# Performance work log

Measured on AMD Instinct MI355X. Metric: run time of the kernel, lower is better.

The kernel has to match this reference:

```python
import jax, jax.numpy as jnp
import numpy as np

N_NODES = 50000
N_EDGES = 600000
N_GRAPHS = 64
IN_D, HID, EMB = 5, 128, 64
BN_EPS = 1e-5


def setup_inputs() -> dict:
    key = jax.random.key(0)
    ks = jax.random.split(key, 16)
    x = jax.random.normal(ks[0], (N_NODES, IN_D), dtype=jnp.float32)
    src = jax.random.randint(ks[1], (N_EDGES,), 0, N_NODES, dtype=jnp.int32)
    dst = jax.random.randint(ks[2], (N_EDGES,), 0, N_NODES, dtype=jnp.int32)
    batch = jnp.sort(jax.random.randint(ks[3], (N_NODES,), 0, N_GRAPHS, dtype=jnp.int32))
    def lin(k, fi, fo):
        s = 1.0 / np.sqrt(fi)
        kw, kb = jax.random.split(k)
        return (jax.random.uniform(kw, (fi, fo), jnp.float32, -s, s),
                jax.random.uniform(kb, (fo,), jnp.float32, -s, s))
    W1, b1 = lin(ks[4], IN_D, HID)
    W2, b2 = lin(ks[5], HID, HID)
    W3, b3 = lin(ks[6], HID, HID)
    Wp, bp = lin(ks[7], HID, EMB)
    g1 = 1.0 + 0.1 * jax.random.normal(ks[8], (HID,), jnp.float32)
    g2 = 1.0 + 0.1 * jax.random.normal(ks[9], (HID,), jnp.float32)
    g3 = 1.0 + 0.1 * jax.random.normal(ks[10], (HID,), jnp.float32)
    be1 = 0.1 * jax.random.normal(ks[11], (HID,), jnp.float32)
    be2 = 0.1 * jax.random.normal(ks[12], (HID,), jnp.float32)
    be3 = 0.1 * jax.random.normal(ks[13], (HID,), jnp.float32)
    return dict(x=x, src=src, dst=dst, batch=batch,
                W1=W1, b1=b1, W2=W2, b2=b2, W3=W3, b3=b3,
                g1=g1, be1=be1, g2=g2, be2=be2, g3=g3, be3=be3,
                Wp=Wp, bp=bp)


def reference(x, src, dst, batch, W1, b1, W2, b2, W3, b3,
              g1, be1, g2, be2, g3, be3, Wp, bp):
    n = x.shape[0]
    # GCNConv with self-loops and symmetric normalization (PyG default)
    loop = jnp.arange(n, dtype=src.dtype)
    s = jnp.concatenate([src, loop])
    d = jnp.concatenate([dst, loop])
    deg = jax.ops.segment_sum(jnp.ones_like(d, dtype=x.dtype), d, num_segments=n)
    dinv = jnp.where(deg > 0, jax.lax.rsqrt(deg), 0.0)
    norm = (dinv[s] * dinv[d])[:, None]  # (E+N, 1)

    def gcn(h, W, b):
        hw = h @ W                                   # (N, HID)
        msg = hw[s] * norm                           # gather + scale
        agg = jax.ops.segment_sum(msg, d, num_segments=n)
        return agg + b

    def bn_relu(h, g, be):
        # eval-mode BatchNorm1d with running_mean=0, running_var=1
        return jax.nn.relu(h * (g * jax.lax.rsqrt(jnp.asarray(1.0 + BN_EPS, h.dtype))) + be)

    h = bn_relu(gcn(x, W1, b1), g1, be1)
    h = bn_relu(gcn(h, W2, b2), g2, be2)
    h = bn_relu(gcn(h, W3, b3), g3, be3)

    # global mean pool over graphs
    sums = jax.ops.segment_sum(h, batch, num_segments=N_GRAPHS)
    cnt = jax.ops.segment_sum(jnp.ones((n,), h.dtype), batch, num_segments=N_GRAPHS)
    pooled = sums / jnp.maximum(cnt, 1.0)[:, None]
    return pooled @ Wp + bp
```

## Files before the change

### kernel.cpp

```cpp
#include <hip/hip_runtime.h>
#include <hip/hip_fp16.h>

#define N_NODES 50000
#define N_EDGES 600000
#define N_GRAPHS 64
#define IN_D 5
#define HID 128
#define EMB 64

#define CHUNK 512
#define NCHUNK ((N_NODES + CHUNK - 1) / CHUNK)
#define NREP 16
#define NLOC 4
#define TB 16
#define ECAP 1024

typedef _Float16 half8 __attribute__((ext_vector_type(8)));
typedef float float4v __attribute__((ext_vector_type(4)));
typedef float floatx2 __attribute__((ext_vector_type(2)));


__global__ __launch_bounds__(256) void k_init(
        int* __restrict__ cnt, float* __restrict__ psum_rep,
        const float* __restrict__ W2, const float* __restrict__ W3,
        _Float16* __restrict__ Wt2, _Float16* __restrict__ Wt3,
        int2* __restrict__ e_pack,
        const float* __restrict__ x, float* __restrict__ xp) {
    int tid = blockIdx.x * blockDim.x + threadIdx.x;
    int nt = gridDim.x * blockDim.x;
    for (int i = tid; i < N_NODES; i += nt) cnt[i] = 0;
    for (int i = tid; i < NREP * N_GRAPHS * HID; i += nt) psum_rep[i] = 0.f;
    if (tid < 8) e_pack[N_EDGES + tid] = make_int2(0, 0);
    for (int i = tid; i < N_NODES * 8; i += nt) {
        int f = i & 7, n = i >> 3;
        xp[i] = (f < IN_D) ? x[n * IN_D + f] : 0.f;
    }
    for (int i = tid; i < 2 * HID * HID; i += nt) {
        int rem = i & (HID * HID - 1);
        int k = rem & 127, f = rem >> 7;
        if (i < HID * HID) Wt2[rem] = (_Float16)W2[k * HID + f];
        else               Wt3[rem] = (_Float16)W3[k * HID + f];
    }
}


__global__ __launch_bounds__(256) void k_count(
        const int* __restrict__ dst, int* __restrict__ cnt) {
    int e = blockIdx.x * blockDim.x + threadIdx.x;
    if (e < N_EDGES) atomicAdd(&cnt[dst[e]], 1);
}


__global__ void k_chunksum(const int* __restrict__ cnt, int* __restrict__ csum,
                           float* __restrict__ dinv) {
    __shared__ int sh[256];
    int b = blockIdx.x, t = threadIdx.x;
    int i0 = b * CHUNK + t, i1 = i0 + 256;
    int v = 0;
    if (i0 < N_NODES) { int c = cnt[i0]; v += c; dinv[i0] = rsqrtf((float)c + 1.0f); }
    if (i1 < N_NODES) { int c = cnt[i1]; v += c; dinv[i1] = rsqrtf((float)c + 1.0f); }
    sh[t] = v; __syncthreads();
    for (int off = 128; off > 0; off >>= 1) {
        if (t < off) sh[t] += sh[t + off];
        __syncthreads();
    }
    if (t == 0) csum[b] = sh[0];
}


__global__ void k_scan(const int* __restrict__ cnt, const int* __restrict__ csum,
                       int* __restrict__ row_start) {
    __shared__ int ws[4];
    int b = blockIdx.x, t = threadIdx.x;
    int lane = t & 63, w = t >> 6;

    int pre = 0;
    for (int j = lane; j < b; j += 64) pre += csum[j];
    #pragma unroll
    for (int off = 32; off > 0; off >>= 1) pre += __shfl_down(pre, off);
    pre = __shfl(pre, 0);

    int base = b * CHUNK;
    int i0 = base + 2 * t, i1 = i0 + 1;
    int c0 = (i0 < N_NODES) ? cnt[i0] : 0;
    int c1 = (i1 < N_NODES) ? cnt[i1] : 0;
    int v = c0 + c1;
    int s = v;
    #pragma unroll
    for (int off = 1; off < 64; off <<= 1) {
        int u = __shfl_up(s, off);
        if (lane >= off) s += u;
    }
    if (lane == 63) ws[w] = s;
    __syncthreads();
    if (t == 0) {
        int r = 0;
        #pragma unroll
        for (int j = 0; j < 4; ++j) { int xx = ws[j]; ws[j] = r; r += xx; }
    }
    __syncthreads();
    int excl = s - v + ws[w] + pre;
    if (i0 < N_NODES) row_start[i0] = excl;
    if (i1 < N_NODES) row_start[i1] = excl + c0;
    if (b == 0 && t == 0) row_start[N_NODES] = N_EDGES;
}


__global__ __launch_bounds__(256) void k_scatter(
        const int* __restrict__ src, const int* __restrict__ dst,
        const float* __restrict__ dinv, const int* __restrict__ row_start,
        int* __restrict__ cnt, int2* __restrict__ e_pack) {
    int e = blockIdx.x * blockDim.x + threadIdx.x;
    if (e >= N_EDGES) return;
    int d = dst[e];
    int pos = row_start[d] + atomicSub(&cnt[d], 1) - 1;
    int s = src[e];
    e_pack[pos] = make_int2(s, __float_as_int(dinv[s]));
}


__global__ __launch_bounds__(256) void k_agg1(
        const float* __restrict__ xp, const float* __restrict__ dinv,
        const int* __restrict__ row_start, const int2* __restrict__ e_pack,
        const float* __restrict__ W1, const float* __restrict__ b1,
        const float* __restrict__ g1, const float* __restrict__ be1,
        unsigned short* __restrict__ H8u) {
    __shared__ int2 eL[ECAP];
    int t = threadIdx.x;
    int w = t >> 6, lane = t & 63;
    int slot8 = lane >> 3, q8 = lane & 7;
    int nb = blockIdx.x * TB;

    int E0 = row_start[nb], E1 = row_start[nb + TB];
    int cntL = E1 - E0 + 8; if (cntL > ECAP) cntL = ECAP;
    for (int i = t; i < cntL; i += 256) eL[i] = e_pack[E0 + i];
    __syncthreads();

    const float rs = rsqrtf(1.0f + 1e-5f);
    int fa = lane * 2, fb = fa + 1;
    float w1a[IN_D], w1b[IN_D];
    #pragma unroll
    for (int k = 0; k < IN_D; ++k) {
        w1a[k] = W1[k * HID + fa];
        w1b[k] = W1[k * HID + fb];
    }
    float b1a = b1[fa], b1b = b1[fb];
    float g1a = g1[fa] * rs, g1b = g1[fb] * rs;
    float e1a = be1[fa], e1b = be1[fb];

    #pragma unroll 1
    for (int i = 0; i < 4; ++i) {
        int n = nb + w * 4 + i;
        int beg = row_start[n], end = row_start[n + 1];
        float acc = 0.f;
        for (int e = beg; e < end; e += 8) {
            int eo = e + slot8 - E0;
            int2 pe;
            if (eo < cntL) pe = eL[eo];
            else           pe = e_pack[e + slot8];
            float fw = (e + slot8 < end) ? __int_as_float(pe.y) : 0.f;
            float g = xp[(size_t)pe.x * 8 + q8];
            acc = fmaf(fw, g, acc);
        }
        acc += __shfl_xor(acc, 8);
        acc += __shfl_xor(acc, 16);
        acc += __shfl_xor(acc, 32);
        float di = dinv[n];
        float av = di * fmaf(di, xp[(size_t)n * 8 + q8], acc);
        float a0 = __shfl(av, 0), a1 = __shfl(av, 1), a2 = __shfl(av, 2),
              a3 = __shfl(av, 3), a4 = __shfl(av, 4);
        float va = b1a, vb = b1b;
        va = fmaf(a0, w1a[0], va); vb = fmaf(a0, w1b[0], vb);
        va = fmaf(a1, w1a[1], va); vb = fmaf(a1, w1b[1], vb);
        va = fmaf(a2, w1a[2], va); vb = fmaf(a2, w1b[2], vb);
        va = fmaf(a3, w1a[3], va); vb = fmaf(a3, w1b[3], vb);
        va = fmaf(a4, w1a[4], va); vb = fmaf(a4, w1b[4], vb);
        va = fmaf(va, g1a, e1a);
        vb = fmaf(vb, g1b, e1b);
        va = va > 0.f ? va : 0.f;
        vb = vb > 0.f ? vb : 0.f;
        int p = __builtin_amdgcn_cvt_pk_fp8_f32(va, vb, 0, false);
        H8u[(size_t)n * 64 + lane] = (unsigned short)(p & 0xffff);
    }
}


__device__ __forceinline__ void agg_node_fp8(
        const unsigned int* __restrict__ H8, const float* __restrict__ dinv,
        const int* __restrict__ row_start, const int2* __restrict__ e_pack,
        const int2* __restrict__ eL, int E0, int cntL,
        int n, int slot8, int q8, _Float16* __restrict__ asrow) {
    float acc[16];
    #pragma unroll
    for (int j = 0; j < 16; ++j) acc[j] = 0.f;
    int beg = row_start[n], end = row_start[n + 1];
    for (int e = beg; e < end; e += 8) {
        int eo = e + slot8 - E0;
        int2 pe;
        if (eo < cntL) pe = eL[eo];
        else           pe = e_pack[e + slot8];
        float fw = (e + slot8 < end) ? __int_as_float(pe.y) : 0.f;
        uint4 g = ((const uint4*)(H8 + (size_t)pe.x * 32))[q8];
        unsigned int gw[4] = {g.x, g.y, g.z, g.w};
        #pragma unroll
        for (int q = 0; q < 4; ++q) {
            floatx2 lo = __builtin_amdgcn_cvt_pk_f32_fp8(gw[q], false);
            floatx2 hi = __builtin_amdgcn_cvt_pk_f32_fp8(gw[q], true);
            acc[4 * q + 0] = fmaf(fw, lo[0], acc[4 * q + 0]);
            acc[4 * q + 1] = fmaf(fw, lo[1], acc[4 * q + 1]);
            acc[4 * q + 2] = fmaf(fw, hi[0], acc[4 * q + 2]);
            acc[4 * q + 3] = fmaf(fw, hi[1], acc[4 * q + 3]);
        }
    }
    #pragma unroll
    for (int j = 0; j < 16; ++j) {
        float a = acc[j];
        a += __shfl_xor(a, 8);
        a += __shfl_xor(a, 16);
        a += __shfl_xor(a, 32);
        acc[j] = a;
    }
    if (slot8 == 0) {
        float di = dinv[n];
        uint4 s = ((const uint4*)(H8 + (size_t)n * 32))[q8];
        unsigned int sw[4] = {s.x, s.y, s.z, s.w};
        float sv[16];
        #pragma unroll
        for (int q = 0; q < 4; ++q) {
            floatx2 lo = __builtin_amdgcn_cvt_pk_f32_fp8(sw[q], false);
            floatx2 hi = __builtin_amdgcn_cvt_pk_f32_fp8(sw[q], true);
            sv[4 * q + 0] = lo[0]; sv[4 * q + 1] = lo[1];
            sv[4 * q + 2] = hi[0]; sv[4 * q + 3] = hi[1];
        }
        half8 o0, o1;
        #pragma unroll
        for (int j = 0; j < 8; ++j)
            o0[j] = (_Float16)(di * fmaf(di, sv[j], acc[j]));
        #pragma unroll
        for (int j = 0; j < 8; ++j)
            o1[j] = (_Float16)(di * fmaf(di, sv[j + 8], acc[j + 8]));
        *(half8*)(asrow + q8 * 16) = o0;
        *(half8*)(asrow + q8 * 16 + 8) = o1;
    }
}


__global__ __launch_bounds__(256) void k_fuse2(
        const unsigned int* __restrict__ Hin, const float* __restrict__ dinv,
        const int* __restrict__ row_start, const int2* __restrict__ e_pack,
        const _Float16* __restrict__ Wt,
        const float* __restrict__ bb, const float* __restrict__ gg,
        const float* __restrict__ bee, unsigned char* __restrict__ out8) {
    __shared__ __align__(16) _Float16 As[TB][136];
    __shared__ int2 eL[ECAP];
    int t = threadIdx.x;
    int w = t >> 6, lane = t & 63;
    int slot8 = lane >> 3, q8 = lane & 7;
    int nb = blockIdx.x * TB;

    int E0 = row_start[nb], E1 = row_start[nb + TB];
    int cntL = E1 - E0 + 8; if (cntL > ECAP) cntL = ECAP;
    for (int i = t; i < cntL; i += 256) eL[i] = e_pack[E0 + i];
    __syncthreads();

    #pragma unroll 1
    for (int i = 0; i < 4; ++i)
        agg_node_fp8(Hin, dinv, row_start, e_pack, eL, E0, cntL,
                     nb + w * 4 + i, slot8, q8, &As[w * 4 + i][0]);
    __syncthreads();

    int quad = lane >> 4, r16 = lane & 15;
    half8 a[4];
    #pragma unroll
    for (int kb = 0; kb < 4; ++kb)
        a[kb] = *(const half8*)&As[r16][(kb * 4 + quad) * 8];
    const float rs = rsqrtf(1.0f + 1e-5f);
    #pragma unroll
    for (int fi = 0; fi < 2; ++fi) {
        int f = (w * 2 + fi) * 16 + r16;
        const half8* Brow = (const half8*)(Wt + (size_t)f * 128);
        float4v acc = {0.f, 0.f, 0.f, 0.f};
        #pragma unroll
        for (int kb = 0; kb < 4; ++kb)
            acc = __builtin_amdgcn_mfma_f32_16x16x32_f16(a[kb], Brow[kb * 4 + quad],
                                                         acc, 0, 0, 0);
        float b0 = bb[f], gf = gg[f] * rs, e0 = bee[f];
        #pragma unroll
        for (int rr = 0; rr < 4; ++rr) {
            float v = fmaf(acc[rr] + b0, gf, e0);
            v = v > 0.f ? v : 0.f;
            int p = __builtin_amdgcn_cvt_pk_fp8_f32(v, 0.f, 0, false);
            out8[(size_t)(nb + quad * 4 + rr) * 128 + f] = (unsigned char)(p & 0xff);
        }
    }
}


__global__ __launch_bounds__(256) void k_fuse3(
        const unsigned int* __restrict__ Hin, const float* __restrict__ dinv,
        const int* __restrict__ row_start, const int2* __restrict__ e_pack,
        const _Float16* __restrict__ Wt,
        const float* __restrict__ bb, const float* __restrict__ gg,
        const float* __restrict__ bee, const int* __restrict__ batch,
        float* __restrict__ psum_rep) {
    __shared__ __align__(16) _Float16 As[TB][136];
    __shared__ int2 eL[ECAP];
    __shared__ float sh_pool[NLOC][HID];
    int t = threadIdx.x;
    int w = t >> 6, lane = t & 63;
    int slot8 = lane >> 3, q8 = lane & 7;
    int blk = (int)blockIdx.x;
    int nb = blk * TB;

    for (int i = t; i < NLOC * HID; i += 256) ((float*)sh_pool)[i] = 0.f;
    int E0 = row_start[nb], E1 = row_start[nb + TB];
    int cntL = E1 - E0 + 8; if (cntL > ECAP) cntL = ECAP;
    for (int i = t; i < cntL; i += 256) eL[i] = e_pack[E0 + i];
    __syncthreads();

    #pragma unroll 1
    for (int i = 0; i < 4; ++i)
        agg_node_fp8(Hin, dinv, row_start, e_pack, eL, E0, cntL,
                     nb + w * 4 + i, slot8, q8, &As[w * 4 + i][0]);

    int quad = lane >> 4, r16 = lane & 15;
    int g0 = batch[nb];
    int gi4[4];
    #pragma unroll
    for (int rr = 0; rr < 4; ++rr) gi4[rr] = batch[nb + quad * 4 + rr];
    __syncthreads();

    half8 a[4];
    #pragma unroll
    for (int kb = 0; kb < 4; ++kb)
        a[kb] = *(const half8*)&As[r16][(kb * 4 + quad) * 8];
    float* rep = psum_rep + (size_t)(blk & (NREP - 1)) * N_GRAPHS * HID;
    const float rs = rsqrtf(1.0f + 1e-5f);
    #pragma unroll
    for (int fi = 0; fi < 2; ++fi) {
        int f = (w * 2 + fi) * 16 + r16;
        const half8* Brow = (const half8*)(Wt + (size_t)f * 128);
        float4v acc = {0.f, 0.f, 0.f, 0.f};
        #pragma unroll
        for (int kb = 0; kb < 4; ++kb)
            acc = __builtin_amdgcn_mfma_f32_16x16x32_f16(a[kb], Brow[kb * 4 + quad],
                                                         acc, 0, 0, 0);
        float b0 = bb[f], gf = gg[f] * rs, e0 = bee[f];
        float partial = 0.f;
        int cur = -1;
        #pragma unroll
        for (int rr = 0; rr < 4; ++rr) {
            float v = fmaf(acc[rr] + b0, gf, e0);
            v = v > 0.f ? v : 0.f;
            int gi = gi4[rr];
            if (gi != cur) {
                if (cur >= 0) {
                    int idx = cur - g0;
                    if (idx < NLOC) atomicAdd(&sh_pool[idx][f], partial);
                    else            atomicAdd(&rep[cur * HID + f], partial);
                }
                partial = 0.f; cur = gi;
            }
            partial += v;
        }
        if (cur >= 0) {
            int idx = cur - g0;
            if (idx < NLOC) atomicAdd(&sh_pool[idx][f], partial);
            else            atomicAdd(&rep[cur * HID + f], partial);
        }
    }
    __syncthreads();
    for (int i = t; i < NLOC * HID; i += 256) {
        int idx = i >> 7, ff = i & 127;
        float v = sh_pool[idx][ff];
        int g = g0 + idx;
        if (v != 0.f && g < N_GRAPHS) atomicAdd(&rep[g * HID + ff], v);
    }
}


__device__ __forceinline__ int lower_bound_batch(const int* __restrict__ batch, int val) {
    int lo = 0, hi = N_NODES;
    while (lo < hi) {
        int mid = (lo + hi) >> 1;
        if (batch[mid] < val) lo = mid + 1;
        else hi = mid;
    }
    return lo;
}

__global__ void k_final(const float* __restrict__ psum_rep, const int* __restrict__ batch,
                        const float* __restrict__ Wp, const float* __restrict__ bp,
                        float* __restrict__ out) {
    __shared__ float s_p[HID];
    int gi = blockIdx.x, e = threadIdx.x;
    for (int f = e; f < HID; f += EMB) {
        float v = 0.f;
        #pragma unroll
        for (int r = 0; r < NREP; ++r)
            v += psum_rep[(size_t)r * N_GRAPHS * HID + gi * HID + f];
        s_p[f] = v;
    }
    int lane = e & 63;
    int r = 0;
    if (lane < 2) r = lower_bound_batch(batch, gi + lane);
    int c0 = __shfl(r, 0), c1 = __shfl(r, 1);
    float inv = 1.0f / fmaxf((float)(c1 - c0), 1.0f);
    __syncthreads();
    float acc = bp[e];
    #pragma unroll 8
    for (int f = 0; f < HID; ++f)
        acc = fmaf(s_p[f] * inv, Wp[f * EMB + e], acc);
    out[gi * EMB + e] = acc;
}


extern "C" void kernel_launch(void* const* d_in, const int* in_sizes, int n_in,
                              void* d_out, int out_size, void* d_ws, size_t ws_size,
                              hipStream_t stream) {
    const float* x   = (const float*)d_in[0];
    const int*   src = (const int*)d_in[1];
    const int*   dst = (const int*)d_in[2];
    const int* batch = (const int*)d_in[3];
    const float* W1 = (const float*)d_in[4];
    const float* b1 = (const float*)d_in[5];
    const float* W2 = (const float*)d_in[6];
    const float* b2 = (const float*)d_in[7];
    const float* W3 = (const float*)d_in[8];
    const float* b3 = (const float*)d_in[9];
    const float* g1 = (const float*)d_in[10];
    const float* be1 = (const float*)d_in[11];
    const float* g2 = (const float*)d_in[12];
    const float* be2 = (const float*)d_in[13];
    const float* g3 = (const float*)d_in[14];
    const float* be3 = (const float*)d_in[15];
    const float* Wp = (const float*)d_in[16];
    const float* bp = (const float*)d_in[17];
    float* out = (float*)d_out;

    char* ws = (char*)d_ws;
    size_t o = 0;
    auto alloc = [&](size_t bytes) {
        void* pp = ws + o;
        o += bytes;
        o = (o + 255) & ~255ull;
        return pp;
    };
    int*      cnt       = (int*)alloc(N_NODES * 4);
    int*      row_start = (int*)alloc((N_NODES + 1) * 4);
    int*      csum      = (int*)alloc(NCHUNK * 4);
    float*    dinv      = (float*)alloc(N_NODES * 4);
    int2*     e_pack    = (int2*)alloc((size_t)(N_EDGES + 8) * 8);
    _Float16* Wt2       = (_Float16*)alloc(HID * HID * 2);
    _Float16* Wt3       = (_Float16*)alloc(HID * HID * 2);
    float*    xp        = (float*)alloc((size_t)N_NODES * 8 * 4);
    unsigned int* H8a   = (unsigned int*)alloc((size_t)N_NODES * HID);
    unsigned int* H8b   = (unsigned int*)alloc((size_t)N_NODES * HID);
    float*    psum_rep  = (float*)alloc((size_t)NREP * N_GRAPHS * HID * 4);

    k_init<<<512, 256, 0, stream>>>(cnt, psum_rep, W2, W3, Wt2, Wt3, e_pack, x, xp);
    k_count<<<(N_EDGES + 255) / 256, 256, 0, stream>>>(dst, cnt);
    k_chunksum<<<NCHUNK, 256, 0, stream>>>(cnt, csum, dinv);
    k_scan<<<NCHUNK, 256, 0, stream>>>(cnt, csum, row_start);
    k_scatter<<<(N_EDGES + 255) / 256, 256, 0, stream>>>(src, dst, dinv, row_start,
                                                         cnt, e_pack);
    k_agg1<<<N_NODES / TB, 256, 0, stream>>>(xp, dinv, row_start, e_pack,
                                             W1, b1, g1, be1, (unsigned short*)H8a);
    k_fuse2<<<N_NODES / TB, 256, 0, stream>>>(H8a, dinv, row_start, e_pack, Wt2,
                                              b2, g2, be2, (unsigned char*)H8b);
    k_fuse3<<<N_NODES / TB, 256, 0, stream>>>(H8b, dinv, row_start, e_pack, Wt3,
                                              b3, g3, be3, batch, psum_rep);
    k_final<<<N_GRAPHS, EMB, 0, stream>>>(psum_rep, batch, Wp, bp, out);
}
```

Baseline: 270.6 us.

## Pack edge records into 32 bits with fp16 weight and drop LDS edge staging

Each CSR edge entry now stores the 16-bit source index and an fp16 copy of dinv[src] in one 32-bit word instead of an int2. This halves edge-list memory traffic in the three aggregation kernels. The shared-memory staging of each block's edge range and its barrier are removed, and edges are read directly from global memory. The cost is reduced precision on the normalisation weight and a hard limit of 65536 nodes.

```diff
diff --git a/kernel.cpp b/kernel.cpp
--- a/kernel.cpp
+++ b/kernel.cpp
@@ -13,24 +13,28 @@
 #define NREP 16
 #define NLOC 4
 #define TB 16
-#define ECAP 1024
 
 typedef _Float16 half8 __attribute__((ext_vector_type(8)));
 typedef float float4v __attribute__((ext_vector_type(4)));
 typedef float floatx2 __attribute__((ext_vector_type(2)));
+
+__device__ __forceinline__ float ep_w(unsigned pe) {
+    return (float)__ushort_as_half((unsigned short)(pe >> 16));
+}
+__device__ __forceinline__ unsigned ep_s(unsigned pe) { return pe & 0xffffu; }
 
 
 __global__ __launch_bounds__(256) void k_init(
         int* __restrict__ cnt, float* __restrict__ psum_rep,
         const float* __restrict__ W2, const float* __restrict__ W3,
         _Float16* __restrict__ Wt2, _Float16* __restrict__ Wt3,
-        int2* __restrict__ e_pack,
+        unsigned int* __restrict__ e_pack,
         const float* __restrict__ x, float* __restrict__ xp) {
     int tid = blockIdx.x * blockDim.x + threadIdx.x;
     int nt = gridDim.x * blockDim.x;
     for (int i = tid; i < N_NODES; i += nt) cnt[i] = 0;
     for (int i = tid; i < NREP * N_GRAPHS * HID; i += nt) psum_rep[i] = 0.f;
-    if (tid < 8) e_pack[N_EDGES + tid] = make_int2(0, 0);
+    if (tid < 8) e_pack[N_EDGES + tid] = 0u;
     for (int i = tid; i < N_NODES * 8; i += nt) {
         int f = i & 7, n = i >> 3;
         xp[i] = (f < IN_D) ? x[n * IN_D + f] : 0.f;
@@ -109,32 +113,27 @@
 __global__ __launch_bounds__(256) void k_scatter(
         const int* __restrict__ src, const int* __restrict__ dst,
         const float* __restrict__ dinv, const int* __restrict__ row_start,
-        int* __restrict__ cnt, int2* __restrict__ e_pack) {
+        int* __restrict__ cnt, unsigned int* __restrict__ e_pack) {
     int e = blockIdx.x * blockDim.x + threadIdx.x;
     if (e >= N_EDGES) return;
     int d = dst[e];
     int pos = row_start[d] + atomicSub(&cnt[d], 1) - 1;
     int s = src[e];
-    e_pack[pos] = make_int2(s, __float_as_int(dinv[s]));
+    unsigned hw = (unsigned)__half_as_ushort(__float2half(dinv[s]));
+    e_pack[pos] = (hw << 16) | (unsigned)s;
 }
 
 
 __global__ __launch_bounds__(256) void k_agg1(
         const float* __restrict__ xp, const float* __restrict__ dinv,
-        const int* __restrict__ row_start, const int2* __restrict__ e_pack,
+        const int* __restrict__ row_start, const unsigned int* __restrict__ e_pack,
         const float* __restrict__ W1, const float* __restrict__ b1,
         const float* __restrict__ g1, const float* __restrict__ be1,
         unsigned short* __restrict__ H8u) {
-    __shared__ int2 eL[ECAP];
     int t = threadIdx.x;
     int w = t >> 6, lane = t & 63;
     int slot8 = lane >> 3, q8 = lane & 7;
     int nb = blockIdx.x * TB;
-
-    int E0 = row_start[nb], E1 = row_start[nb + TB];
-    int cntL = E1 - E0 + 8; if (cntL > ECAP) cntL = ECAP;
-    for (int i = t; i < cntL; i += 256) eL[i] = e_pack[E0 + i];
-    __syncthreads();
 
     const float rs = rsqrtf(1.0f + 1e-5f);
     int fa = lane * 2, fb = fa + 1;
@@ -154,12 +153,9 @@
         int beg = row_start[n], end = row_start[n + 1];
         float acc = 0.f;
         for (int e = beg; e < end; e += 8) {
-            int eo = e + slot8 - E0;
-            int2 pe;
-            if (eo < cntL) pe = eL[eo];
-            else           pe = e_pack[e + slot8];
-            float fw = (e + slot8 < end) ? __int_as_float(pe.y) : 0.f;
-            float g = xp[(size_t)pe.x * 8 + q8];
+            unsigned pe = e_pack[e + slot8];
+            float fw = (e + slot8 < end) ? ep_w(pe) : 0.f;
+            float g = xp[(size_t)ep_s(pe) * 8 + q8];
             acc = fmaf(fw, g, acc);
         }
         acc += __shfl_xor(acc, 8);
@@ -187,20 +183,16 @@
 
 __device__ __forceinline__ void agg_node_fp8(
         const unsigned int* __restrict__ H8, const float* __restrict__ dinv,
-        const int* __restrict__ row_start, const int2* __restrict__ e_pack,
-        const int2* __restrict__ eL, int E0, int cntL,
+        const int* __restrict__ row_start, const unsigned int* __restrict__ e_pack,
         int n, int slot8, int q8, _Float16* __restrict__ asrow) {
     float acc[16];
     #pragma unroll
     for (int j = 0; j < 16; ++j) acc[j] = 0.f;
     int beg = row_start[n], end = row_start[n + 1];
     for (int e = beg; e < end; e += 8) {
-        int eo = e + slot8 - E0;
-        int2 pe;
-        if (eo < cntL) pe = eL[eo];
-        else           pe = e_pack[e + slot8];
-        float fw = (e + slot8 < end) ? __int_as_float(pe.y) : 0.f;
-        uint4 g = ((const uint4*)(H8 + (size_t)pe.x * 32))[q8];
+        unsigned pe = e_pack[e + slot8];
+        float fw = (e + slot8 < end) ? ep_w(pe) : 0.f;
+        uint4 g = ((const uint4*)(H8 + (size_t)ep_s(pe) * 32))[q8];
         unsigned int gw[4] = {g.x, g.y, g.z, g.w};
         #pragma unroll
         for (int q = 0; q < 4; ++q) {
@@ -247,25 +239,19 @@
 
 __global__ __launch_bounds__(256) void k_fuse2(
         const unsigned int* __restrict__ Hin, const float* __restrict__ dinv,
-        const int* __restrict__ row_start, const int2* __restrict__ e_pack,
+        const int* __restrict__ row_start, const unsigned int* __restrict__ e_pack,
         const _Float16* __restrict__ Wt,
         const float* __restrict__ bb, const float* __restrict__ gg,
         const float* __restrict__ bee, unsigned char* __restrict__ out8) {
     __shared__ __align__(16) _Float16 As[TB][136];
-    __shared__ int2 eL[ECAP];
     int t = threadIdx.x;
     int w = t >> 6, lane = t & 63;
     int slot8 = lane >> 3, q8 = lane & 7;
     int nb = blockIdx.x * TB;
 
-    int E0 = row_start[nb], E1 = row_start[nb + TB];
-    int cntL = E1 - E0 + 8; if (cntL > ECAP) cntL = ECAP;
-    for (int i = t; i < cntL; i += 256) eL[i] = e_pack[E0 + i];
-    __syncthreads();
-
     #pragma unroll 1
     for (int i = 0; i < 4; ++i)
-        agg_node_fp8(Hin, dinv, row_start, e_pack, eL, E0, cntL,
+        agg_node_fp8(Hin, dinv, row_start, e_pack,
                      nb + w * 4 + i, slot8, q8, &As[w * 4 + i][0]);
     __syncthreads();
 
@@ -298,13 +284,12 @@
 
 __global__ __launch_bounds__(256) void k_fuse3(
         const unsigned int* __restrict__ Hin, const float* __restrict__ dinv,
-        const int* __restrict__ row_start, const int2* __restrict__ e_pack,
+        const int* __restrict__ row_start, const unsigned int* __restrict__ e_pack,
         const _Float16* __restrict__ Wt,
         const float* __restrict__ bb, const float* __restrict__ gg,
         const float* __restrict__ bee, const int* __restrict__ batch,
         float* __restrict__ psum_rep) {
     __shared__ __align__(16) _Float16 As[TB][136];
-    __shared__ int2 eL[ECAP];
     __shared__ float sh_pool[NLOC][HID];
     int t = threadIdx.x;
     int w = t >> 6, lane = t & 63;
@@ -313,14 +298,11 @@
     int nb = blk * TB;
 
     for (int i = t; i < NLOC * HID; i += 256) ((float*)sh_pool)[i] = 0.f;
-    int E0 = row_start[nb], E1 = row_start[nb + TB];
-    int cntL = E1 - E0 + 8; if (cntL > ECAP) cntL = ECAP;
-    for (int i = t; i < cntL; i += 256) eL[i] = e_pack[E0 + i];
     __syncthreads();
 
     #pragma unroll 1
     for (int i = 0; i < 4; ++i)
-        agg_node_fp8(Hin, dinv, row_start, e_pack, eL, E0, cntL,
+        agg_node_fp8(Hin, dinv, row_start, e_pack,
                      nb + w * 4 + i, slot8, q8, &As[w * 4 + i][0]);
 
     int quad = lane >> 4, r16 = lane & 15;
@@ -450,7 +432,7 @@
     int*      row_start = (int*)alloc((N_NODES + 1) * 4);
     int*      csum      = (int*)alloc(NCHUNK * 4);
     float*    dinv      = (float*)alloc(N_NODES * 4);
-    int2*     e_pack    = (int2*)alloc((size_t)(N_EDGES + 8) * 8);
+    unsigned int* e_pack = (unsigned int*)alloc((size_t)(N_EDGES + 8) * 4);
     _Float16* Wt2       = (_Float16*)alloc(HID * HID * 2);
     _Float16* Wt3       = (_Float16*)alloc(HID * HID * 2);
     float*    xp        = (float*)alloc((size_t)N_NODES * 8 * 4);
```

Result: no change. 270.7 us (+0.0%).
